# Performance work log

Hardware: AMD Instinct MI355X
Metric: run time of the kernel (lower is better)

The kernel has to match this reference:

```python
import math
import jax, jax.numpy as jnp
import numpy as np

B, S, D = 4, 2048, 1024
N_HEAD = 16


def setup_inputs() -> dict:
    key = jax.random.key(0)
    k1, k2 = jax.random.split(key)
    x = jax.random.normal(k1, (B, S, D), dtype=jnp.float32)
    # xavier-uniform style scale for the fused QKV kernel
    limit = math.sqrt(6.0 / (D + 3 * D))
    W_qkv = jax.random.uniform(k2, (D, 3 * D), dtype=jnp.float32, minval=-limit, maxval=limit)
    b_qkv = jnp.zeros((3 * D,), dtype=jnp.float32)
    return {"x": x, "W_qkv": W_qkv, "b_qkv": b_qkv}


def reference(x, W_qkv, b_qkv):
    batch_size, seq_len, d_model = x.shape
    head_dim = d_model // N_HEAD
    # fused QKV projection: [B, S, 3D]
    qkv = jnp.einsum('bsd,de->bse', x, W_qkv) + b_qkv
    qkv = qkv.reshape(batch_size, seq_len, N_HEAD, 3 * head_dim)
    qkv = qkv.transpose(0, 2, 1, 3)  # [B, H, S, 3*hd]
    q, k, v = jnp.split(qkv, 3, axis=-1)
    # scaled dot-product attention with causal mask
    attn_logits = jnp.einsum('bhqd,bhkd->bhqk', q, k) / math.sqrt(head_dim)
    causal = jnp.tril(jnp.ones((seq_len, seq_len), dtype=jnp.float32))[None, None]
    attn_logits = jnp.where(causal == 0, -jnp.inf, attn_logits)
    attn = jax.nn.softmax(attn_logits, axis=-1)
    out = jnp.einsum('bhqk,bhkd->bhqd', attn, v)  # [B, H, S, hd]
    out = out.transpose(0, 2, 1, 3).reshape(batch_size, seq_len, -1)
    return out
```

## Files before the change

kernel.cpp:

```cpp
#include <hip/hip_runtime.h>
#include <hip/hip_bf16.h>
#include <cstdint>

typedef __bf16 bf16x8 __attribute__((ext_vector_type(8)));
typedef float f32x4 __attribute__((ext_vector_type(4)));

__device__ inline unsigned short f2bf(float f) {
    union { float f; unsigned int u; } v; v.f = f;
    unsigned int u = v.u;
    unsigned int r = (u + 0x7FFFu + ((u >> 16) & 1u)) >> 16;
    return (unsigned short)r;
}

__device__ inline f32x4 mfma16(bf16x8 a, bf16x8 b, f32x4 c) {
    return __builtin_amdgcn_mfma_f32_16x16x32_bf16(a, b, c, 0, 0, 0);
}

__device__ inline bf16x8 ldfrag(const unsigned short* p) {
    uint4 v = *(const uint4*)p;
    return __builtin_bit_cast(bf16x8, v);
}

__device__ inline void cp16(const unsigned short* g, unsigned short* l) {
    __builtin_amdgcn_global_load_lds(
        (const __attribute__((address_space(1))) unsigned int*)g,
        (__attribute__((address_space(3))) unsigned int*)l,
        16, 0, 0);
}

__device__ inline unsigned int pkbf(float a, float b) {
    return __builtin_amdgcn_perm(__builtin_bit_cast(unsigned int, b),
                                 __builtin_bit_cast(unsigned int, a),
                                 0x07060302u);
}

__global__ void k_convert_x(const float* __restrict__ in,
                            unsigned short* __restrict__ out, int n4) {
    int i = blockIdx.x * blockDim.x + threadIdx.x;
    if (i < n4) {
        float4 f = ((const float4*)in)[i];
        ushort4 o;
        o.x = f2bf(f.x); o.y = f2bf(f.y); o.z = f2bf(f.z); o.w = f2bf(f.w);
        ((ushort4*)out)[i] = o;
    }
}

__global__ void k_transpose_w(const float* __restrict__ W,
                              unsigned short* __restrict__ Wt) {
    __shared__ float tile[32][33];
    int nt = blockIdx.x, kt = blockIdx.y;
    int tx = threadIdx.x & 31, ty = threadIdx.x >> 5;
#pragma unroll
    for (int yy = 0; yy < 4; ++yy) {
        int y = ty + yy * 8;
        tile[y][tx] = W[(size_t)(kt * 32 + y) * 3072 + nt * 32 + tx];
    }
    __syncthreads();
#pragma unroll
    for (int yy = 0; yy < 4; ++yy) {
        int nrow = ty + yy * 8;
        Wt[(size_t)(nt * 32 + nrow) * 1024 + kt * 32 + tx] = f2bf(tile[tx][nrow]);
    }
}

__global__ __launch_bounds__(256) void k_qkv_gemm(
    const unsigned short* __restrict__ A,
    const unsigned short* __restrict__ Bt,
    const float* __restrict__ bias,
    unsigned short* __restrict__ C) {
    __shared__ unsigned short As[128 * 32];
    __shared__ unsigned short Bs[128 * 32];
    const int tid = threadIdx.x;
    const int lane = tid & 63;
    const int w = tid >> 6;
    const int wm = w >> 1, wn = w & 1;
    const int l15 = lane & 15;
    const int quad = lane >> 4;
    const int m0 = blockIdx.y * 128;
    const int n0 = blockIdx.x * 128;

    f32x4 acc[4][4] = {};

    for (int k0 = 0; k0 < 1024; k0 += 32) {
#pragma unroll
        for (int i = 0; i < 2; ++i) {
            int c = tid + i * 256;
            int row = c >> 2, seg = c & 3;
            cp16(A + (size_t)(m0 + row) * 1024 + k0 + seg * 8, &As[c * 8]);
            cp16(Bt + (size_t)(n0 + row) * 1024 + k0 + seg * 8, &Bs[c * 8]);
        }
        __syncthreads();
        const int col8 = quad * 8;
        bf16x8 af[4], bfr[4];
#pragma unroll
        for (int i = 0; i < 4; ++i)
            af[i] = ldfrag(As + (wm * 64 + i * 16 + l15) * 32 + col8);
#pragma unroll
        for (int j = 0; j < 4; ++j)
            bfr[j] = ldfrag(Bs + (wn * 64 + j * 16 + l15) * 32 + col8);
#pragma unroll
        for (int i = 0; i < 4; ++i)
#pragma unroll
            for (int j = 0; j < 4; ++j)
                acc[i][j] = mfma16(af[i], bfr[j], acc[i][j]);
        __syncthreads();
    }
#pragma unroll
    for (int i = 0; i < 4; ++i) {
#pragma unroll
        for (int j = 0; j < 4; ++j) {
            int col = n0 + wn * 64 + j * 16 + l15;
            float bv = bias[col];
#pragma unroll
            for (int r = 0; r < 4; ++r) {
                int row = m0 + wm * 64 + i * 16 + quad * 4 + r;
                C[(size_t)row * 3072 + col] = f2bf(acc[i][j][r] + bv);
            }
        }
    }
}

__global__ __launch_bounds__(256) void k_transpose_v(
    const unsigned short* __restrict__ qkv,
    unsigned short* __restrict__ VtG) {
    __shared__ unsigned short t[64][65];
    const int st = blockIdx.x;
    const int h = blockIdx.y;
    const int b = blockIdx.z;
    const int tid = threadIdx.x;
    const int voff = h * 192 + 128;
    const size_t base = (size_t)b * 2048 * 3072;
#pragma unroll
    for (int i = 0; i < 2; ++i) {
        int c = tid + i * 256;
        int row = c >> 3, seg = c & 7;
        uint4 v = *(const uint4*)(qkv + base + (size_t)(st * 64 + row) * 3072 + voff + seg * 8);
        unsigned short u8[8];
        *(uint4*)u8 = v;
#pragma unroll
        for (int u = 0; u < 8; ++u) t[row][seg * 8 + u] = u8[u];
    }
    __syncthreads();
    const size_t obase = ((size_t)(b * 16 + h) * 64) * 2048 + st * 64;
#pragma unroll
    for (int i = 0; i < 2; ++i) {
        int c = tid + i * 256;
        int drow = c >> 3, seg = c & 7;
        unsigned short u8[8];
#pragma unroll
        for (int u = 0; u < 8; ++u) u8[u] = t[seg * 8 + u][drow];
        *(uint4*)(VtG + obase + (size_t)drow * 2048 + seg * 8) = *(uint4*)u8;
    }
}

__global__ __launch_bounds__(256) void k_attn(
    const unsigned short* __restrict__ qkv,
    const unsigned short* __restrict__ VtG,
    float* __restrict__ out) {
    const int p = blockIdx.x;
    const int hb = p & 63;
    const int h = hb & 15;
    const int b = hb >> 4;
    const int qt_hi = 31 - (p >> 6);
    const int qt_lo = p >> 6;
    const int tid = threadIdx.x;
    const int lane = tid & 63;
    const int w = tid >> 6;
    const int l15 = lane & 15;
    const int quad = lane >> 4;

    __shared__ unsigned short KsF[2 * 64 * 64];
    __shared__ unsigned short VsF[2 * 64 * 64];
    __shared__ unsigned short PsF[4 * 16 * 64];

    const size_t base = (size_t)b * 2048 * 3072;
    const int qoff = h * 192, koff = h * 192 + 64;
    const size_t vtbase = (size_t)(b * 16 + h) * 64 * 2048;

    const int srow0 = tid >> 3, sseg = tid & 7;
    const int swz8 = (sseg ^ (srow0 & 7)) * 8;
    unsigned short* kd0 = &KsF[srow0 * 64 + swz8];
    unsigned short* kd1 = &KsF[(srow0 + 32) * 64 + swz8];
    unsigned short* vd0 = &VsF[srow0 * 64 + swz8];
    unsigned short* vd1 = &VsF[(srow0 + 32) * 64 + swz8];

    const int xr = l15 & 7;
    const int rb0 = (quad ^ xr) * 8;
    const int rb1 = ((quad + 4) ^ xr) * 8;

    const float sc = 0.125f * 1.44269504088896340736f;
    const int pwbase = w * 1024 + l15 * 64;
    unsigned short* prd = &PsF[pwbase];

    auto run_item = [&](int qt) {
        const int qbw = qt * 64 + w * 16;
        const unsigned short* qp =
            qkv + base + (size_t)(qbw + l15) * 3072 + qoff + quad * 8;
        const bf16x8 bq0 = ldfrag(qp);
        const bf16x8 bq1 = ldfrag(qp + 32);

        const unsigned short* kp0 = qkv + base + koff + sseg * 8 + (size_t)srow0 * 3072;
        const unsigned short* kp1 = kp0 + (size_t)32 * 3072;
        const unsigned short* vp0 = VtG + vtbase + (size_t)srow0 * 2048 + sseg * 8;
        const unsigned short* vp1 = vp0 + (size_t)32 * 2048;

        f32x4 o[4] = {};
        float ptot = 0.f;

        uint4 kr0 = *(const uint4*)kp0;
        uint4 kr1 = *(const uint4*)kp1;
        uint4 vr0 = *(const uint4*)vp0;
        uint4 vr1 = *(const uint4*)vp1;

        __syncthreads();

        for (int kt = 0; kt <= qt; ++kt) {
            const int bo = (kt & 1) * 4096;
            *(uint4*)(kd0 + bo) = kr0;
            *(uint4*)(kd1 + bo) = kr1;
            *(uint4*)(vd0 + bo) = vr0;
            *(uint4*)(vd1 + bo) = vr1;
            if (kt < qt) {
                kp0 += 64 * 3072; kp1 += 64 * 3072;
                vp0 += 64;        vp1 += 64;
                kr0 = *(const uint4*)kp0;
                kr1 = *(const uint4*)kp1;
                vr0 = *(const uint4*)vp0;
                vr1 = *(const uint4*)vp1;
            }
            __syncthreads();

            f32x4 s[4];
#pragma unroll
            for (int j = 0; j < 4; ++j) {
                const unsigned short* kr = &KsF[bo + (j * 16 + l15) * 64];
                f32x4 z = {0.f, 0.f, 0.f, 0.f};
                z = mfma16(ldfrag(kr + rb0), bq0, z);
                z = mfma16(ldfrag(kr + rb1), bq1, z);
                s[j] = z;
            }

            if (kt == qt) {
                const int qrel = w * 16 + l15;
#pragma unroll
                for (int j = 0; j < 4; ++j) {
                    const int sb = j * 16 + quad * 4;
#pragma unroll
                    for (int r = 0; r < 4; ++r)
                        if (sb + r > qrel) s[j][r] = -3.0e38f;
                }
            }

#pragma unroll
            for (int j = 0; j < 4; ++j) {
                float pv[4];
#pragma unroll
                for (int r = 0; r < 4; ++r) {
                    pv[r] = __builtin_amdgcn_exp2f(
                        __builtin_fmaf(s[j][r], sc, -16.0f));
                    ptot += pv[r];
                }
                unsigned int lo = pkbf(pv[0], pv[1]);
                unsigned int hi = pkbf(pv[2], pv[3]);
                const int sblk = (j * 2 + (quad >> 1)) ^ xr;
                uint2 pk; pk.x = lo; pk.y = hi;
                *(uint2*)&PsF[pwbase + sblk * 8 + (quad & 1) * 4] = pk;
            }

            bf16x8 bp0 = ldfrag(prd + rb0);
            bf16x8 bp1 = ldfrag(prd + rb1);
#pragma unroll
            for (int jd = 0; jd < 4; ++jd) {
                const unsigned short* vr = &VsF[bo + (jd * 16 + l15) * 64];
                o[jd] = mfma16(ldfrag(vr + rb0), bp0, o[jd]);
                o[jd] = mfma16(ldfrag(vr + rb1), bp1, o[jd]);
            }
        }

        float l = ptot;
        l += __shfl_xor(l, 16, 64);
        l += __shfl_xor(l, 32, 64);
        const float inv = __builtin_amdgcn_rcpf(l);
        float* op = out + ((size_t)b * 2048 + qbw + l15) * 1024 + h * 64 + quad * 4;
#pragma unroll
        for (int jd = 0; jd < 4; ++jd) {
            float4 v;
            v.x = o[jd][0] * inv; v.y = o[jd][1] * inv;
            v.z = o[jd][2] * inv; v.w = o[jd][3] * inv;
            *(float4*)(op + jd * 16) = v;
        }
    };

    run_item(qt_hi);
    run_item(qt_lo);
}

extern "C" void kernel_launch(void* const* d_in, const int* in_sizes, int n_in,
                              void* d_out, int out_size, void* d_ws, size_t ws_size,
                              hipStream_t stream) {
    const float* x = (const float*)d_in[0];
    const float* W = (const float*)d_in[1];
    const float* bq = (const float*)d_in[2];
    float* out = (float*)d_out;

    unsigned short* xbf = (unsigned short*)d_ws;
    unsigned short* wtbf = xbf + (size_t)8192 * 1024;
    unsigned short* qkvbf = wtbf + (size_t)3072 * 1024;
    unsigned short* VtG = xbf;

    k_convert_x<<<8192, 256, 0, stream>>>(x, xbf, 8192 * 1024 / 4);
    k_transpose_w<<<dim3(96, 32), 256, 0, stream>>>(W, wtbf);
    k_qkv_gemm<<<dim3(24, 64), 256, 0, stream>>>(xbf, wtbf, bq, qkvbf);
    k_transpose_v<<<dim3(32, 16, 4), 256, 0, stream>>>(qkvbf, VtG);
    k_attn<<<1024, 256, 0, stream>>>(qkvbf, VtG, out);
}
```

Measured before the change: 228.4 us.

## Use 32x32 MFMA with register-resident P and async LDS loads in attention

Rewrites the attention inner loop around 32x32x16 bf16 MFMAs, with warps split 2x2 over key rows and query columns. The P tile now stays in registers via permlane32 swaps, removing the LDS round trip and its scratch buffer. K and V are copied straight into double-buffered LDS with global_load_lds instead of passing through registers. Because the key dimension is split across warp pairs, partial outputs and row sums must be reduced through LDS at the end of each item, which adds an extra barrier and some epilogue traffic.

Measured after the change: 230.4 us. Within noise of the previous version (+0.9%).

```diff
diff --git a/kernel.cpp b/kernel.cpp
--- a/kernel.cpp
+++ b/kernel.cpp
@@ -4,6 +4,7 @@
 
 typedef __bf16 bf16x8 __attribute__((ext_vector_type(8)));
 typedef float f32x4 __attribute__((ext_vector_type(4)));
+typedef float f32x16 __attribute__((ext_vector_type(16)));
 
 __device__ inline unsigned short f2bf(float f) {
     union { float f; unsigned int u; } v; v.f = f;
@@ -16,6 +17,10 @@
     return __builtin_amdgcn_mfma_f32_16x16x32_bf16(a, b, c, 0, 0, 0);
 }
 
+__device__ inline f32x16 mfma32(bf16x8 a, bf16x8 b, f32x16 c) {
+    return __builtin_amdgcn_mfma_f32_32x32x16_bf16(a, b, c, 0, 0, 0);
+}
+
 __device__ inline bf16x8 ldfrag(const unsigned short* p) {
     uint4 v = *(const uint4*)p;
     return __builtin_bit_cast(bf16x8, v);
@@ -32,6 +37,12 @@
     return __builtin_amdgcn_perm(__builtin_bit_cast(unsigned int, b),
                                  __builtin_bit_cast(unsigned int, a),
                                  0x07060302u);
+}
+
+__device__ inline void plswap(unsigned int& a, unsigned int& b) {
+    typedef unsigned int u32x2 __attribute__((ext_vector_type(2)));
+    u32x2 r = __builtin_amdgcn_permlane32_swap(a, b, false, false);
+    a = r[0]; b = r[1];
 }
 
 __global__ void k_convert_x(const float* __restrict__ in,
@@ -166,129 +177,160 @@
     const int tid = threadIdx.x;
     const int lane = tid & 63;
     const int w = tid >> 6;
-    const int l15 = lane & 15;
-    const int quad = lane >> 4;
-
-    __shared__ unsigned short KsF[2 * 64 * 64];
-    __shared__ unsigned short VsF[2 * 64 * 64];
-    __shared__ unsigned short PsF[4 * 16 * 64];
+    const int wm = w >> 1;
+    const int wn = w & 1;
+    const int l31 = lane & 31;
+    const int hi = lane >> 5;
+
+    __shared__ __align__(16) unsigned short KsF[2 * 64 * 64];
+    __shared__ __align__(16) unsigned short VsF[2 * 64 * 64];
 
     const size_t base = (size_t)b * 2048 * 3072;
     const int qoff = h * 192, koff = h * 192 + 64;
     const size_t vtbase = (size_t)(b * 16 + h) * 64 * 2048;
 
     const int srow0 = tid >> 3, sseg = tid & 7;
-    const int swz8 = (sseg ^ (srow0 & 7)) * 8;
-    unsigned short* kd0 = &KsF[srow0 * 64 + swz8];
-    unsigned short* kd1 = &KsF[(srow0 + 32) * 64 + swz8];
-    unsigned short* vd0 = &VsF[srow0 * 64 + swz8];
-    unsigned short* vd1 = &VsF[(srow0 + 32) * 64 + swz8];
-
-    const int xr = l15 & 7;
-    const int rb0 = (quad ^ xr) * 8;
-    const int rb1 = ((quad + 4) ^ xr) * 8;
+    const int gsw = (sseg ^ (srow0 & 7)) * 8;
+    unsigned short* kd0 = &KsF[tid * 8];
+    unsigned short* kd1 = &KsF[2048 + tid * 8];
+    unsigned short* vd0 = &VsF[tid * 8];
+    unsigned short* vd1 = &VsF[2048 + tid * 8];
+
+    const int xr7 = l31 & 7;
+    const int kfbase = (32 * wm + l31) * 64;
+    const int vfb0 = l31 * 64;
+    const int vfb1 = (32 + l31) * 64;
+    const int qcol = 32 * wn + l31;
 
     const float sc = 0.125f * 1.44269504088896340736f;
-    const int pwbase = w * 1024 + l15 * 64;
-    unsigned short* prd = &PsF[pwbase];
 
     auto run_item = [&](int qt) {
-        const int qbw = qt * 64 + w * 16;
-        const unsigned short* qp =
-            qkv + base + (size_t)(qbw + l15) * 3072 + qoff + quad * 8;
-        const bf16x8 bq0 = ldfrag(qp);
-        const bf16x8 bq1 = ldfrag(qp + 32);
-
-        const unsigned short* kp0 = qkv + base + koff + sseg * 8 + (size_t)srow0 * 3072;
+        const int qrow = qt * 64 + qcol;
+        const unsigned short* qp = qkv + base + (size_t)qrow * 3072 + qoff + hi * 8;
+        bf16x8 bq[4];
+#pragma unroll
+        for (int t = 0; t < 4; ++t) bq[t] = ldfrag(qp + t * 16);
+
+        const unsigned short* kp0 = qkv + base + koff + (size_t)srow0 * 3072 + gsw;
         const unsigned short* kp1 = kp0 + (size_t)32 * 3072;
-        const unsigned short* vp0 = VtG + vtbase + (size_t)srow0 * 2048 + sseg * 8;
+        const unsigned short* vp0 = VtG + vtbase + (size_t)srow0 * 2048 + gsw;
         const unsigned short* vp1 = vp0 + (size_t)32 * 2048;
 
-        f32x4 o[4] = {};
+        f32x16 acc0 = {0,0,0,0,0,0,0,0,0,0,0,0,0,0,0,0};
+        f32x16 acc1 = {0,0,0,0,0,0,0,0,0,0,0,0,0,0,0,0};
         float ptot = 0.f;
 
-        uint4 kr0 = *(const uint4*)kp0;
-        uint4 kr1 = *(const uint4*)kp1;
-        uint4 vr0 = *(const uint4*)vp0;
-        uint4 vr1 = *(const uint4*)vp1;
-
+        cp16(kp0, kd0); cp16(kp1, kd1); cp16(vp0, vd0); cp16(vp1, vd1);
         __syncthreads();
 
         for (int kt = 0; kt <= qt; ++kt) {
             const int bo = (kt & 1) * 4096;
-            *(uint4*)(kd0 + bo) = kr0;
-            *(uint4*)(kd1 + bo) = kr1;
-            *(uint4*)(vd0 + bo) = vr0;
-            *(uint4*)(vd1 + bo) = vr1;
+            const int bn = bo ^ 4096;
             if (kt < qt) {
                 kp0 += 64 * 3072; kp1 += 64 * 3072;
                 vp0 += 64;        vp1 += 64;
-                kr0 = *(const uint4*)kp0;
-                kr1 = *(const uint4*)kp1;
-                vr0 = *(const uint4*)vp0;
-                vr1 = *(const uint4*)vp1;
-            }
+                cp16(kp0, kd0 + bn); cp16(kp1, kd1 + bn);
+                cp16(vp0, vd0 + bn); cp16(vp1, vd1 + bn);
+            }
+
+            f32x16 s = {0,0,0,0,0,0,0,0,0,0,0,0,0,0,0,0};
+#pragma unroll
+            for (int t = 0; t < 4; ++t) {
+                const unsigned short* ka =
+                    &KsF[bo + kfbase + ((2 * t + hi) ^ xr7) * 8];
+                s = mfma32(ldfrag(ka), bq[t], s);
+            }
+
+            if (kt == qt) {
+#pragma unroll
+                for (int r = 0; r < 16; ++r) {
+                    const int srow = 32 * wm + (r & 3) + 8 * (r >> 2) + 4 * hi;
+                    if (srow > qcol) s[r] = -3.0e38f;
+                }
+            }
+
+            float pvv[16];
+#pragma unroll
+            for (int r = 0; r < 16; ++r) {
+                pvv[r] = __builtin_amdgcn_exp2f(
+                    __builtin_fmaf(s[r], sc, -16.0f));
+                ptot += pvv[r];
+            }
+            unsigned int pk0 = pkbf(pvv[0], pvv[1]),   pk1 = pkbf(pvv[2], pvv[3]);
+            unsigned int pk2 = pkbf(pvv[4], pvv[5]),   pk3 = pkbf(pvv[6], pvv[7]);
+            unsigned int pk4 = pkbf(pvv[8], pvv[9]),   pk5 = pkbf(pvv[10], pvv[11]);
+            unsigned int pk6 = pkbf(pvv[12], pvv[13]), pk7 = pkbf(pvv[14], pvv[15]);
+            plswap(pk0, pk2); plswap(pk1, pk3);
+            plswap(pk4, pk6); plswap(pk5, pk7);
+            uint4 w0; w0.x = pk0; w0.y = pk1; w0.z = pk2; w0.w = pk3;
+            uint4 w1; w1.x = pk4; w1.y = pk5; w1.z = pk6; w1.w = pk7;
+            const bf16x8 pf0 = __builtin_bit_cast(bf16x8, w0);
+            const bf16x8 pf1 = __builtin_bit_cast(bf16x8, w1);
+
+            const int su0 = ((4 * wm + hi) ^ xr7) * 8;
+            const int su1 = ((4 * wm + 2 + hi) ^ xr7) * 8;
+            acc0 = mfma32(ldfrag(&VsF[bo + vfb0 + su0]), pf0, acc0);
+            acc0 = mfma32(ldfrag(&VsF[bo + vfb0 + su1]), pf1, acc0);
+            acc1 = mfma32(ldfrag(&VsF[bo + vfb1 + su0]), pf0, acc1);
+            acc1 = mfma32(ldfrag(&VsF[bo + vfb1 + su1]), pf1, acc1);
+
             __syncthreads();
-
-            f32x4 s[4];
-#pragma unroll
-            for (int j = 0; j < 4; ++j) {
-                const unsigned short* kr = &KsF[bo + (j * 16 + l15) * 64];
-                f32x4 z = {0.f, 0.f, 0.f, 0.f};
-                z = mfma16(ldfrag(kr + rb0), bq0, z);
-                z = mfma16(ldfrag(kr + rb1), bq1, z);
-                s[j] = z;
-            }
-
-            if (kt == qt) {
-                const int qrel = w * 16 + l15;
-#pragma unroll
-                for (int j = 0; j < 4; ++j) {
-                    const int sb = j * 16 + quad * 4;
-#pragma unroll
-                    for (int r = 0; r < 4; ++r)
-                        if (sb + r > qrel) s[j][r] = -3.0e38f;
-                }
-            }
-
-#pragma unroll
-            for (int j = 0; j < 4; ++j) {
-                float pv[4];
-#pragma unroll
-                for (int r = 0; r < 4; ++r) {
-                    pv[r] = __builtin_amdgcn_exp2f(
-                        __builtin_fmaf(s[j][r], sc, -16.0f));
-                    ptot += pv[r];
-                }
-                unsigned int lo = pkbf(pv[0], pv[1]);
-                unsigned int hi = pkbf(pv[2], pv[3]);
-                const int sblk = (j * 2 + (quad >> 1)) ^ xr;
-                uint2 pk; pk.x = lo; pk.y = hi;
-                *(uint2*)&PsF[pwbase + sblk * 8 + (quad & 1) * 4] = pk;
-            }
-
-            bf16x8 bp0 = ldfrag(prd + rb0);
-            bf16x8 bp1 = ldfrag(prd + rb1);
-#pragma unroll
-            for (int jd = 0; jd < 4; ++jd) {
-                const unsigned short* vr = &VsF[bo + (jd * 16 + l15) * 64];
-                o[jd] = mfma16(ldfrag(vr + rb0), bp0, o[jd]);
-                o[jd] = mfma16(ldfrag(vr + rb1), bp1, o[jd]);
-            }
-        }
-
-        float l = ptot;
-        l += __shfl_xor(l, 16, 64);
-        l += __shfl_xor(l, 32, 64);
-        const float inv = __builtin_amdgcn_rcpf(l);
-        float* op = out + ((size_t)b * 2048 + qbw + l15) * 1024 + h * 64 + quad * 4;
-#pragma unroll
-        for (int jd = 0; jd < 4; ++jd) {
-            float4 v;
-            v.x = o[jd][0] * inv; v.y = o[jd][1] * inv;
-            v.z = o[jd][2] * inv; v.w = o[jd][3] * inv;
-            *(float4*)(op + jd * 16) = v;
-        }
+        }
+
+        float* Sc = (float*)KsF;
+        float* Pt = (float*)VsF;
+        const int lb = (wn * 64 + lane) * 8;
+        if (wm == 1) {
+#pragma unroll
+            for (int g = 0; g < 4; ++g) {
+                float4 v;
+                v.x = acc0[g * 4 + 0]; v.y = acc0[g * 4 + 1];
+                v.z = acc0[g * 4 + 2]; v.w = acc0[g * 4 + 3];
+                ((float4*)Sc)[lb + (g ^ (lane & 7))] = v;
+            }
+#pragma unroll
+            for (int g = 0; g < 4; ++g) {
+                float4 v;
+                v.x = acc1[g * 4 + 0]; v.y = acc1[g * 4 + 1];
+                v.z = acc1[g * 4 + 2]; v.w = acc1[g * 4 + 3];
+                ((float4*)Sc)[lb + ((g + 4) ^ (lane & 7))] = v;
+            }
+            Pt[wn * 64 + lane] = ptot;
+        }
+        __syncthreads();
+        if (wm == 0) {
+#pragma unroll
+            for (int g = 0; g < 4; ++g) {
+                float4 v = ((const float4*)Sc)[lb + (g ^ (lane & 7))];
+                acc0[g * 4 + 0] += v.x; acc0[g * 4 + 1] += v.y;
+                acc0[g * 4 + 2] += v.z; acc0[g * 4 + 3] += v.w;
+            }
+#pragma unroll
+            for (int g = 0; g < 4; ++g) {
+                float4 v = ((const float4*)Sc)[lb + ((g + 4) ^ (lane & 7))];
+                acc1[g * 4 + 0] += v.x; acc1[g * 4 + 1] += v.y;
+                acc1[g * 4 + 2] += v.z; acc1[g * 4 + 3] += v.w;
+            }
+            float l = ptot + Pt[wn * 64 + lane];
+            l += __shfl_xor(l, 32, 64);
+            const float inv = __builtin_amdgcn_rcpf(l);
+            float* op = out + ((size_t)b * 2048 + qrow) * 1024 + h * 64 + 4 * hi;
+#pragma unroll
+            for (int g = 0; g < 4; ++g) {
+                float4 v;
+                v.x = acc0[g * 4 + 0] * inv; v.y = acc0[g * 4 + 1] * inv;
+                v.z = acc0[g * 4 + 2] * inv; v.w = acc0[g * 4 + 3] * inv;
+                *(float4*)(op + g * 8) = v;
+            }
+#pragma unroll
+            for (int g = 0; g < 4; ++g) {
+                float4 v;
+                v.x = acc1[g * 4 + 0] * inv; v.y = acc1[g * 4 + 1] * inv;
+                v.z = acc1[g * 4 + 2] * inv; v.w = acc1[g * 4 + 3] * inv;
+                *(float4*)(op + 32 + g * 8) = v;
+            }
+        }
+        __syncthreads();
     };
 
     run_item(qt_hi);
```
